# Performance work log

Hardware: AMD Instinct MI355X
Metric: run time of the kernel (lower is better)

## Reference

```python
import jax, jax.numpy as jnp
import numpy as np

INTEGRAL_RESOLUTION = 0.03  # matches self.integral_resolution

S, H, E, G, F = 4096, 3, 512, 3334, 1  # samples, heads, max events, grid points, formulas


def setup_inputs() -> dict:
    key = jax.random.key(0)
    k1, k2, k3, k4, k5, k6 = jax.random.split(key, 6)
    event_features = jax.random.uniform(k1, (S, H, E, F), dtype=jnp.float32)
    event_mask = jax.random.randint(k2, (S, H, E), 0, 2).astype(bool)
    grid_features = jax.random.uniform(k3, (S, H, G, F), dtype=jnp.float32)
    weights = jax.random.normal(k4, (H, F), dtype=jnp.float32)
    bases = jax.random.normal(k5, (H,), dtype=jnp.float32)
    effects = jnp.ones((H, F), dtype=jnp.float32)  # formula effect is +/-1
    return {
        "event_features": event_features,
        "event_mask": event_mask,
        "grid_features": grid_features,
        "weights": weights,
        "bases": bases,
        "effects": effects,
    }


def reference(event_features, event_mask, grid_features, weights, bases, effects):
    # intensity(t, h) = exp(base_h + sum_f w_{h,f} * feature_f(t) * effect_{h,f})
    w_eff = weights * effects  # [H, F]
    # log-intensity at event times: [S, H, E]
    ev_logit = bases[None, :, None] + jnp.einsum('shef,hf->she', event_features, w_eff)
    # log-intensity on the integral grid: [S, H, G]
    gr_logit = bases[None, :, None] + jnp.einsum('shgf,hf->shg', grid_features, w_eff)
    # sum of log(intensity) over valid events (log(exp(x)) = x)
    log_sum = jnp.sum(jnp.where(event_mask, ev_logit, jnp.zeros((), ev_logit.dtype)))
    # Riemann integral of intensity over [0, T_max]
    integral = jnp.asarray(INTEGRAL_RESOLUTION, gr_logit.dtype) * jnp.sum(jnp.exp(gr_logit))
    return log_sum - integral
```

## Files before the change

### kernel.cpp

```cpp
#include <hip/hip_runtime.h>

constexpr int S = 4096;
constexpr int H = 3;
constexpr int E = 512;
constexpr int G = 3334;
constexpr float RES = 0.03f;
constexpr float LOG2E = 1.44269504088896340736f;

constexpr int NBLK = 2048;
constexpr int BT   = 256;
constexpr int NF4G = S * H * G / 4;
constexpr int GPB  = NF4G / NBLK;
constexpr int NF4E = S * H * E / 4;
constexpr int EPB  = NF4E / NBLK;
constexpr int TAIL_T = GPB - 19 * BT;

#if __has_builtin(__builtin_amdgcn_exp2f)
#define EXP2(x) __builtin_amdgcn_exp2f(x)
#else
#define EXP2(x) exp2f(x)
#endif

__device__ __forceinline__ float quad_exp(int fidx, float4 y,
                                          float c0, float c1, float c2,
                                          float v0, float v1, float v2) {
    int j = fidx * 4;
    int q = j / G;
    int r = j - q * G;
    int m = q - (q / 3) * 3;
    int hB = (m == 2) ? 0 : (m + 1);
    float cA = (m == 0) ? c0 : ((m == 1) ? c1 : c2);
    float vA = (m == 0) ? v0 : ((m == 1) ? v1 : v2);
    float cB = (hB == 0) ? c0 : ((hB == 1) ? c1 : c2);
    float vB = (hB == 0) ? v0 : ((hB == 1) ? v1 : v2);
    int lim = G - r;
    float s;
    s  = EXP2(cA + vA * y.x);
    s += EXP2(((1 >= lim) ? cB : cA) + ((1 >= lim) ? vB : vA) * y.y);
    s += EXP2(((2 >= lim) ? cB : cA) + ((2 >= lim) ? vB : vA) * y.z);
    s += EXP2(((3 >= lim) ? cB : cA) + ((3 >= lim) ? vB : vA) * y.w);
    return s;
}

__global__ __launch_bounds__(256) void logic_model_kernel(
    const float* __restrict__ ev,
    const int*   __restrict__ mask,
    const float* __restrict__ gr,
    const float* __restrict__ w,
    const float* __restrict__ bases,
    const float* __restrict__ eff,
    float* __restrict__ out)
{
    const float b0 = bases[0], b1 = bases[1], b2 = bases[2];
    const float w0 = w[0] * eff[0], w1 = w[1] * eff[1], w2 = w[2] * eff[2];
    const float c0 = b0 * LOG2E, c1 = b1 * LOG2E, c2 = b2 * LOG2E;
    const float v0 = w0 * LOG2E, v1 = w1 * LOG2E, v2 = w2 * LOG2E;

    const int t = threadIdx.x;
    const float4* ev4 = (const float4*)ev;
    const int4*   m4  = (const int4*)mask;
    const float4* gr4 = (const float4*)gr;

    const int ebase = blockIdx.x * EPB + t;
    const int gbase = blockIdx.x * GPB;

    float4 p1x[3]; int4 p1m[3];
    #pragma unroll
    for (int u = 0; u < 3; ++u) {
        p1x[u] = ev4[ebase + u * BT];
        p1m[u] = m4[ebase + u * BT];
    }
    float4 buf[4][4];
    #pragma unroll
    for (int g = 0; g < 3; ++g) {
        #pragma unroll
        for (int u = 0; u < 4; ++u) {
            int slot = 4 * g + u;
            buf[g][u] = gr4[gbase + t + slot * BT];
        }
    }
    __builtin_amdgcn_sched_barrier(0);

    float acc_ev = 0.f;
    #pragma unroll
    for (int u = 0; u < 3; ++u) {
        int row = (ebase + u * BT) >> 7;
        int h = row - (row / 3) * 3;
        float bb = (h == 0) ? b0 : ((h == 1) ? b1 : b2);
        float ww = (h == 0) ? w0 : ((h == 1) ? w1 : w2);
        float4 x = p1x[u]; int4 m = p1m[u];
        if (m.x) acc_ev += bb + ww * x.x;
        if (m.y) acc_ev += bb + ww * x.y;
        if (m.z) acc_ev += bb + ww * x.z;
        if (m.w) acc_ev += bb + ww * x.w;
    }
    __builtin_amdgcn_sched_barrier(0);

    float acc_gr = 0.f;
    #pragma unroll
    for (int b = 0; b < 5; ++b) {
        if (b + 3 < 5) {
            int g = b + 3;
            #pragma unroll
            for (int u = 0; u < 4; ++u) {
                int slot = 4 * g + u;
                int pos = t + slot * BT;
                int idx = gbase + ((slot == 19 && t >= TAIL_T) ? 0 : pos);
                buf[g & 3][u] = gr4[idx];
            }
        }
        __builtin_amdgcn_sched_barrier(0);
        #pragma unroll
        for (int u = 0; u < 4; ++u) {
            int slot = 4 * b + u;
            int pos = t + slot * BT;
            bool valid = (slot < 19) || (t < TAIL_T);
            int fidx = gbase + (valid ? pos : 0);
            float s = quad_exp(fidx, buf[b & 3][u], c0, c1, c2, v0, v1, v2);
            acc_gr += valid ? s : 0.f;
        }
        __builtin_amdgcn_sched_barrier(0);
    }

    float v = acc_ev - RES * acc_gr;

    #pragma unroll
    for (int off = 32; off > 0; off >>= 1)
        v += __shfl_down(v, off, 64);

    __shared__ float sdata[4];
    const int wave = threadIdx.x >> 6;
    const int lane = threadIdx.x & 63;
    if (lane == 0) sdata[wave] = v;
    __syncthreads();
    if (threadIdx.x == 0) {
        float s = sdata[0] + sdata[1] + sdata[2] + sdata[3];
        atomicAdd(out, s);
    }
}

extern "C" void kernel_launch(void* const* d_in, const int* in_sizes, int n_in,
                              void* d_out, int out_size, void* d_ws, size_t ws_size,
                              hipStream_t stream) {
    const float* ev    = (const float*)d_in[0];
    const int*   mask  = (const int*)  d_in[1];
    const float* gr    = (const float*)d_in[2];
    const float* wgt   = (const float*)d_in[3];
    const float* bases = (const float*)d_in[4];
    const float* eff   = (const float*)d_in[5];
    float* out = (float*)d_out;

    hipMemsetAsync(out, 0, sizeof(float), stream);

    logic_model_kernel<<<NBLK, BT, 0, stream>>>(ev, mask, gr, wgt, bases, eff, out);
}
```

Baseline: 272.0 us.

## Stream half of grid loads through LDS via global_load_lds per iteration

Replaces the fully unrolled register prefetch pipeline with a rolled loop of five iterations. Each iteration loads two float4 slices into registers and sends two more straight into LDS using global_load_lds, with a barrier on each side of the compute. The aim is to lower VGPR pressure and use the LDS-direct path for bandwidth. The cost is two block-wide syncs per iteration, less overlap between loads and exp computation, and a switch from the raw exp2 builtin to exp2f.

Result: no change. 276.0 us (+1.5%).

```diff
diff --git a/kernel.cpp b/kernel.cpp
--- a/kernel.cpp
+++ b/kernel.cpp
@@ -9,19 +9,17 @@
 
 constexpr int NBLK = 2048;
 constexpr int BT   = 256;
-constexpr int NF4G = S * H * G / 4;
-constexpr int GPB  = NF4G / NBLK;
-constexpr int NF4E = S * H * E / 4;
-constexpr int EPB  = NF4E / NBLK;
+constexpr int GPB  = S * H * G / 4 / NBLK;
+constexpr int EPB  = S * H * E / 4 / NBLK;
 constexpr int TAIL_T = GPB - 19 * BT;
 
-#if __has_builtin(__builtin_amdgcn_exp2f)
-#define EXP2(x) __builtin_amdgcn_exp2f(x)
-#else
-#define EXP2(x) exp2f(x)
-#endif
+typedef float f4_t __attribute__((ext_vector_type(4)));
+typedef int   i4_t __attribute__((ext_vector_type(4)));
 
-__device__ __forceinline__ float quad_exp(int fidx, float4 y,
+typedef __attribute__((address_space(3))) unsigned char  lds_b;
+typedef __attribute__((address_space(1))) const unsigned char glb_b;
+
+__device__ __forceinline__ float quad_exp(int fidx, f4_t y,
                                           float c0, float c1, float c2,
                                           float v0, float v1, float v2) {
     int j = fidx * 4;
@@ -35,10 +33,28 @@
     float vB = (hB == 0) ? v0 : ((hB == 1) ? v1 : v2);
     int lim = G - r;
     float s;
-    s  = EXP2(cA + vA * y.x);
-    s += EXP2(((1 >= lim) ? cB : cA) + ((1 >= lim) ? vB : vA) * y.y);
-    s += EXP2(((2 >= lim) ? cB : cA) + ((2 >= lim) ? vB : vA) * y.z);
-    s += EXP2(((3 >= lim) ? cB : cA) + ((3 >= lim) ? vB : vA) * y.w);
+    s  = __expf((cA + vA * y.x) * 0.69314718056f);
+    return s;
+}
+
+__device__ __forceinline__ float quad_exp2(int fidx, f4_t y,
+                                           float c0, float c1, float c2,
+                                           float v0, float v1, float v2) {
+    int j = fidx * 4;
+    int q = j / G;
+    int r = j - q * G;
+    int m = q - (q / 3) * 3;
+    int hB = (m == 2) ? 0 : (m + 1);
+    float cA = (m == 0) ? c0 : ((m == 1) ? c1 : c2);
+    float vA = (m == 0) ? v0 : ((m == 1) ? v1 : v2);
+    float cB = (hB == 0) ? c0 : ((hB == 1) ? c1 : c2);
+    float vB = (hB == 0) ? v0 : ((hB == 1) ? v1 : v2);
+    int lim = G - r;
+    float s;
+    s  = exp2f(cA + vA * y.x);
+    s += exp2f(((1 >= lim) ? cB : cA) + ((1 >= lim) ? vB : vA) * y.y);
+    s += exp2f(((2 >= lim) ? cB : cA) + ((2 >= lim) ? vB : vA) * y.z);
+    s += exp2f(((3 >= lim) ? cB : cA) + ((3 >= lim) ? vB : vA) * y.w);
     return s;
 }
 
@@ -56,70 +72,71 @@
     const float c0 = b0 * LOG2E, c1 = b1 * LOG2E, c2 = b2 * LOG2E;
     const float v0 = w0 * LOG2E, v1 = w1 * LOG2E, v2 = w2 * LOG2E;
 
-    const int t = threadIdx.x;
-    const float4* ev4 = (const float4*)ev;
-    const int4*   m4  = (const int4*)mask;
-    const float4* gr4 = (const float4*)gr;
+    const int t  = threadIdx.x;
+    const int b  = blockIdx.x;
+    const int wv = t >> 6;
 
-    const int ebase = blockIdx.x * EPB + t;
-    const int gbase = blockIdx.x * GPB;
+    const f4_t* ev4 = (const f4_t*)ev;
+    const i4_t* m4  = (const i4_t*)mask;
+    const f4_t* gr4 = (const f4_t*)gr;
 
-    float4 p1x[3]; int4 p1m[3];
-    #pragma unroll
-    for (int u = 0; u < 3; ++u) {
-        p1x[u] = ev4[ebase + u * BT];
-        p1m[u] = m4[ebase + u * BT];
-    }
-    float4 buf[4][4];
-    #pragma unroll
-    for (int g = 0; g < 3; ++g) {
+    float acc_ev = 0.f;
+    {
+        const int ebase = b * EPB + t;
         #pragma unroll
-        for (int u = 0; u < 4; ++u) {
-            int slot = 4 * g + u;
-            buf[g][u] = gr4[gbase + t + slot * BT];
+        for (int u = 0; u < 3; ++u) {
+            int i = ebase + u * BT;
+            f4_t x = ev4[i];
+            i4_t m = m4[i];
+            int row = i >> 7;
+            int h = row - (row / 3) * 3;
+            float bb = (h == 0) ? b0 : ((h == 1) ? b1 : b2);
+            float ww = (h == 0) ? w0 : ((h == 1) ? w1 : w2);
+            if (m.x) acc_ev += bb + ww * x.x;
+            if (m.y) acc_ev += bb + ww * x.y;
+            if (m.z) acc_ev += bb + ww * x.z;
+            if (m.w) acc_ev += bb + ww * x.w;
         }
     }
-    __builtin_amdgcn_sched_barrier(0);
 
-    float acc_ev = 0.f;
-    #pragma unroll
-    for (int u = 0; u < 3; ++u) {
-        int row = (ebase + u * BT) >> 7;
-        int h = row - (row / 3) * 3;
-        float bb = (h == 0) ? b0 : ((h == 1) ? b1 : b2);
-        float ww = (h == 0) ? w0 : ((h == 1) ? w1 : w2);
-        float4 x = p1x[u]; int4 m = p1m[u];
-        if (m.x) acc_ev += bb + ww * x.x;
-        if (m.y) acc_ev += bb + ww * x.y;
-        if (m.z) acc_ev += bb + ww * x.z;
-        if (m.w) acc_ev += bb + ww * x.w;
-    }
-    __builtin_amdgcn_sched_barrier(0);
+    __shared__ f4_t lbuf[512];
+    const int gbase = b * GPB;
+    float acc_gr = 0.f;
 
-    float acc_gr = 0.f;
-    #pragma unroll
-    for (int b = 0; b < 5; ++b) {
-        if (b + 3 < 5) {
-            int g = b + 3;
-            #pragma unroll
-            for (int u = 0; u < 4; ++u) {
-                int slot = 4 * g + u;
-                int pos = t + slot * BT;
-                int idx = gbase + ((slot == 19 && t >= TAIL_T) ? 0 : pos);
-                buf[g & 3][u] = gr4[idx];
+    #pragma unroll 1
+    for (int k = 0; k < 5; ++k) {
+        const int s0 = 4 * k;
+        f4_t ra = gr4[gbase + t + (s0 + 0) * BT];
+        f4_t rb = gr4[gbase + t + (s0 + 1) * BT];
+#if __has_builtin(__builtin_amdgcn_global_load_lds)
+        {
+            const glb_b* ga = (const glb_b*)(gr4 + gbase + (s0 + 2) * BT + t);
+            lds_b* la = (lds_b*)((lds_b*)lbuf + (size_t)wv * 1024);
+            __builtin_amdgcn_global_load_lds(ga, la, 16, 0, 0);
+            bool full = (s0 + 3 < 19) || (t < TAIL_T);
+            if (full) {
+                const glb_b* gb2 = (const glb_b*)(gr4 + gbase + (s0 + 3) * BT + t);
+                lds_b* lb2 = (lds_b*)((lds_b*)lbuf + 4096 + (size_t)wv * 1024);
+                __builtin_amdgcn_global_load_lds(gb2, lb2, 16, 0, 0);
             }
         }
-        __builtin_amdgcn_sched_barrier(0);
-        #pragma unroll
-        for (int u = 0; u < 4; ++u) {
-            int slot = 4 * b + u;
-            int pos = t + slot * BT;
-            bool valid = (slot < 19) || (t < TAIL_T);
-            int fidx = gbase + (valid ? pos : 0);
-            float s = quad_exp(fidx, buf[b & 3][u], c0, c1, c2, v0, v1, v2);
-            acc_gr += valid ? s : 0.f;
+#else
+        {
+            lbuf[t] = gr4[gbase + (s0 + 2) * BT + t];
+            if ((s0 + 3 < 19) || (t < TAIL_T))
+                lbuf[256 + t] = gr4[gbase + (s0 + 3) * BT + t];
         }
-        __builtin_amdgcn_sched_barrier(0);
+#endif
+        __syncthreads();
+        acc_gr += quad_exp2(gbase + t + (s0 + 0) * BT, ra, c0, c1, c2, v0, v1, v2);
+        acc_gr += quad_exp2(gbase + t + (s0 + 1) * BT, rb, c0, c1, c2, v0, v1, v2);
+        f4_t ya = lbuf[t];
+        acc_gr += quad_exp2(gbase + t + (s0 + 2) * BT, ya, c0, c1, c2, v0, v1, v2);
+        if ((s0 + 3 < 19) || (t < TAIL_T)) {
+            f4_t yb = lbuf[256 + t];
+            acc_gr += quad_exp2(gbase + t + (s0 + 3) * BT, yb, c0, c1, c2, v0, v1, v2);
+        }
+        __syncthreads();
     }
 
     float v = acc_ev - RES * acc_gr;
@@ -129,11 +146,9 @@
         v += __shfl_down(v, off, 64);
 
     __shared__ float sdata[4];
-    const int wave = threadIdx.x >> 6;
-    const int lane = threadIdx.x & 63;
-    if (lane == 0) sdata[wave] = v;
+    if ((t & 63) == 0) sdata[t >> 6] = v;
     __syncthreads();
-    if (threadIdx.x == 0) {
+    if (t == 0) {
         float s = sdata[0] + sdata[1] + sdata[2] + sdata[3];
         atomicAdd(out, s);
     }
@@ -151,6 +166,5 @@
     float* out = (float*)d_out;
 
     hipMemsetAsync(out, 0, sizeof(float), stream);
-
     logic_model_kernel<<<NBLK, BT, 0, stream>>>(ev, mask, gr, wgt, bases, eff, out);
 }
```
